# Kernel optimization log

Measured on AMD Instinct MI355X. Metric: run time of the kernel, lower is better.

Reference implementation:

```python
import jax, jax.numpy as jnp
import numpy as np
import math

N, NF, D, HEADS, LEVELS, POINTS = 1, 2, 256, 8, 4, 4
SPATIAL = np.array([[100, 100], [50, 50], [25, 25], [13, 13]], dtype=np.int32)
LEN_IN = int((SPATIAL[:, 0] * SPATIAL[:, 1]).sum())  # 13294
LEN_Q = LEN_IN


def _grid_init_bias():
    # faithful to MSDeformAttn._reset_parameters
    thetas = np.arange(HEADS, dtype=np.float32) * (2.0 * math.pi / HEADS)
    grid = np.stack([np.cos(thetas), np.sin(thetas)], -1)
    grid = grid / np.abs(grid).max(-1, keepdims=True)
    grid = np.tile(grid.reshape(HEADS, 1, 1, 2), (1, LEVELS, POINTS, 1))
    for i in range(POINTS):
        grid[:, :, i, :] *= i + 1
    return grid.reshape(-1).astype(np.float32)  # [HEADS*LEVELS*POINTS*2]


def setup_inputs() -> dict:
    key = jax.random.key(0)
    ks = jax.random.split(key, 8)
    lsi = np.concatenate([[0], np.cumsum(SPATIAL[:, 0] * SPATIAL[:, 1])[:-1]]).astype(np.int32)
    s = 1.0 / math.sqrt(D)
    return {
        "query": jax.random.normal(ks[0], (N, NF, LEN_Q, D), jnp.float32),
        "reference_points": jax.random.uniform(ks[1], (N, LEN_Q, LEVELS, 2), jnp.float32),
        "input_flatten": jax.random.normal(ks[2], (N, NF, LEN_IN, D), jnp.float32),
        "input_spatial_shapes": jnp.asarray(SPATIAL),
        "input_level_start_index": jnp.asarray(lsi),
        "Wv": jax.random.normal(ks[3], (D, D), jnp.float32) * s,
        "bv": jnp.zeros((D,), jnp.float32),
        "Woff": jax.random.normal(ks[4], (D, HEADS * LEVELS * POINTS * 2), jnp.float32) * 0.01,
        "boff": jnp.asarray(_grid_init_bias()),
        "Wattn": jax.random.normal(ks[5], (D, HEADS * LEVELS * POINTS), jnp.float32) * 0.02,
        "battn": jnp.zeros((HEADS * LEVELS * POINTS,), jnp.float32),
        "Wout": jax.random.normal(ks[6], (D, D), jnp.float32) * s,
        "bout": jnp.zeros((D,), jnp.float32),
    }


def ms_deform_attn_core(value, spatial_shapes, level_start_index, loc, attn):
    """value: [B, Lin, H, Dh]; loc: [B, Lq, H, L, P, 2] in [0,1]; attn: [B, Lq, H, L, P].
    Bilinear sampling matches F.grid_sample(align_corners=False, padding_mode='zeros')
    applied to grid = 2*loc - 1, i.e. pixel coord = loc*size - 0.5."""
    B, Lin, Hn, Dh = value.shape
    Lq, L, P = loc.shape[1], loc.shape[3], loc.shape[4]
    val_t = value.transpose(0, 2, 1, 3)  # [B, H, Lin, Dh]
    out = jnp.zeros((B, Lq, Hn, Dh), value.dtype)
    for l in range(L):
        Hl = spatial_shapes[l, 0]
        Wl = spatial_shapes[l, 1]
        start = level_start_index[l]
        x = loc[:, :, :, l, :, 0] * Wl - 0.5  # [B, Lq, H, P]
        y = loc[:, :, :, l, :, 1] * Hl - 0.5
        x0 = jnp.floor(x)
        y0 = jnp.floor(y)
        lx, ly = x - x0, y - y0
        x0i = x0.astype(jnp.int32)
        y0i = y0.astype(jnp.int32)
        sampled = jnp.zeros((B, Lq, Hn, P, Dh), value.dtype)
        corners = [(0, 0, (1 - lx) * (1 - ly)), (0, 1, lx * (1 - ly)),
                   (1, 0, (1 - lx) * ly), (1, 1, lx * ly)]
        for dy, dx, w in corners:
            xi = x0i + dx
            yi = y0i + dy
            valid = (xi >= 0) & (xi < Wl) & (yi >= 0) & (yi < Hl)
            idx = start + jnp.clip(yi, 0, Hl - 1) * Wl + jnp.clip(xi, 0, Wl - 1)
            idx_t = idx.transpose(0, 2, 1, 3).reshape(B, Hn, Lq * P)  # [B, H, Lq*P]
            v = jnp.take_along_axis(val_t, idx_t[:, :, :, None], axis=2)  # [B, H, Lq*P, Dh]
            v = v.reshape(B, Hn, Lq, P, Dh).transpose(0, 2, 1, 3, 4)  # [B, Lq, H, P, Dh]
            sampled = sampled + jnp.where(valid, w, 0.0)[..., None] * v
        out = out + jnp.einsum('blhp,blhpd->blhd', attn[:, :, :, l, :], sampled)
    return out.reshape(B, Lq, Hn * Dh)


def reference(query, reference_points, input_flatten, input_spatial_shapes,
              input_level_start_index, Wv, bv, Woff, boff, Wattn, battn, Wout, bout):
    n, nf, Lq, d = query.shape
    Lin = input_flatten.shape[2]
    Dh = d // HEADS
    value = (input_flatten @ Wv + bv).reshape(n * nf, Lin, HEADS, Dh)
    off = (query @ Woff + boff).reshape(n, nf, Lq, HEADS, LEVELS, POINTS, 2)
    aw = (query @ Wattn + battn).reshape(n, nf, Lq, HEADS, LEVELS * POINTS)
    aw = jax.nn.softmax(aw, axis=-1).reshape(n, nf, Lq, HEADS, LEVELS, POINTS)
    # offset normalizer: [W, H] per level
    norm = jnp.stack([input_spatial_shapes[:, 1], input_spatial_shapes[:, 0]], -1).astype(query.dtype)
    # reference_points: [n, Lq, L, 2] -> broadcast with offsets [n, nf, Lq, H, L, P, 2]
    loc = reference_points[:, None, :, None, :, None, :] + off / norm[None, None, None, None, :, None, :]
    loc = loc.reshape(n * nf, Lq, HEADS, LEVELS, POINTS, 2)
    aw = aw.reshape(n * nf, Lq, HEADS, LEVELS, POINTS)
    out = ms_deform_attn_core(value, input_spatial_shapes, input_level_start_index, loc, aw)
    out = out.reshape(n, nf, Lq, d)
    return out @ Wout + bout
```

## Files before the change

### kernel.cpp

```cpp
#include <hip/hip_runtime.h>
#include <math.h>

#define LEN_Q 13294
#define LEN_IN 13294
#define NFRAMES 2
#define MTOT (LEN_Q * NFRAMES)
#define HEADS 8
#define LEVELS 4
#define POINTS 4

typedef __attribute__((ext_vector_type(8))) short short8;
typedef __attribute__((ext_vector_type(4))) float f32x4;
typedef __attribute__((ext_vector_type(4))) int i32x4;
typedef __attribute__((ext_vector_type(2))) unsigned int uint2v;
typedef __attribute__((ext_vector_type(4))) unsigned int uint4v;
typedef __attribute__((ext_vector_type(4))) unsigned short ushort4v;

__device__ __forceinline__ unsigned short f2bf(float x) {
    unsigned u = __builtin_bit_cast(unsigned, x);
    unsigned r = (u + 0x7fffu + ((u >> 16) & 1u)) >> 16;
    return (unsigned short)r;
}
__device__ __forceinline__ float bf2f(unsigned short b) {
    return __builtin_bit_cast(float, (unsigned)b << 16);
}
__device__ __forceinline__ float bfl(unsigned u) {
    return __builtin_bit_cast(float, u << 16);
}
__device__ __forceinline__ float bfh(unsigned u) {
    return __builtin_bit_cast(float, u & 0xffff0000u);
}

#define LSTR 40

__global__ __launch_bounds__(256) void prep_weights(
    const float* __restrict__ Wv,  const float* __restrict__ Woff,
    const float* __restrict__ Wat, const float* __restrict__ Wout,
    unsigned short* __restrict__ wvT,
    unsigned short* __restrict__ woaT,
    unsigned short* __restrict__ woutT)
{
    const int b = blockIdx.x;
    const int k = threadIdx.x;
    const float* src; unsigned short* dst; int N; int n;
    if (b < 256)      { src = Wv;   dst = wvT;          N = 256; n = b; }
    else if (b < 512) { src = Woff; dst = woaT;         N = 256; n = b - 256; }
    else if (b < 640) { src = Wat;  dst = woaT + 65536; N = 128; n = b - 512; }
    else              { src = Wout; dst = woutT;        N = 256; n = b - 640; }
    dst[(size_t)n * 256 + k] = f2bf(src[(size_t)k * N + n]);
}

__global__ __launch_bounds__(256, 3) void gemm_fused(
    const float* __restrict__ Aval,
    const float* __restrict__ Aq,
    const unsigned short* __restrict__ BTv,
    const unsigned short* __restrict__ BToa,
    const float* __restrict__ bv,
    const float* __restrict__ boff,
    const float* __restrict__ battn,
    unsigned short* __restrict__ vdup,
    unsigned short* __restrict__ off16,
    unsigned short* __restrict__ at16,
    int M, int K)
{
    __shared__ unsigned short As[128 * LSTR];
    __shared__ unsigned short Bs[128 * LSTR];

    const int t = threadIdx.x;
    const int w = t >> 6;
    const int L = t & 63;
    const int m0 = blockIdx.y * 128;
    const bool isVal = (blockIdx.x < 2);
    const int nTile = isVal ? blockIdx.x : blockIdx.x - 2;
    const float* Af = isVal ? Aval : Aq;
    const unsigned short* BTb = (isVal ? BTv : BToa) + (size_t)nTile * 128 * K;

    const int sr = t >> 1;
    const int sc = (t & 1) * 16;
    int arow = m0 + sr; if (arow > M - 1) arow = M - 1;
    const float* Ag = Af + (size_t)arow * K + sc;
    const unsigned short* Bg = BTb + (size_t)sr * K + sc;
    unsigned short* AsW = &As[sr * LSTR + sc];
    unsigned short* BsW = &Bs[sr * LSTR + sc];

    const int mq = (w & 1) * 64;
    const int nq = (w >> 1) * 64;
    const int lr = L & 15;
    const int kq = (L >> 4) * 8;

    f32x4 acc[4][4];
    #pragma unroll
    for (int i = 0; i < 4; ++i)
        #pragma unroll
        for (int j = 0; j < 4; ++j) acc[i][j] = (f32x4){0.f, 0.f, 0.f, 0.f};

    f32x4 a0 = *(const f32x4*)(Ag);
    f32x4 a1 = *(const f32x4*)(Ag + 4);
    f32x4 a2 = *(const f32x4*)(Ag + 8);
    f32x4 a3 = *(const f32x4*)(Ag + 12);
    short8 b0 = *(const short8*)(Bg);
    short8 b1 = *(const short8*)(Bg + 8);

    for (int k0 = 0; k0 < K; k0 += 32) {
        short8 p0, p1;
        p0[0]=(short)f2bf(a0.x); p0[1]=(short)f2bf(a0.y); p0[2]=(short)f2bf(a0.z); p0[3]=(short)f2bf(a0.w);
        p0[4]=(short)f2bf(a1.x); p0[5]=(short)f2bf(a1.y); p0[6]=(short)f2bf(a1.z); p0[7]=(short)f2bf(a1.w);
        p1[0]=(short)f2bf(a2.x); p1[1]=(short)f2bf(a2.y); p1[2]=(short)f2bf(a2.z); p1[3]=(short)f2bf(a2.w);
        p1[4]=(short)f2bf(a3.x); p1[5]=(short)f2bf(a3.y); p1[6]=(short)f2bf(a3.z); p1[7]=(short)f2bf(a3.w);
        __syncthreads();
        *(short8*)(AsW) = p0;
        *(short8*)(AsW + 8) = p1;
        *(short8*)(BsW) = b0;
        *(short8*)(BsW + 8) = b1;
        __syncthreads();

        if (k0 + 32 < K) {
            a0 = *(const f32x4*)(Ag + k0 + 32);
            a1 = *(const f32x4*)(Ag + k0 + 36);
            a2 = *(const f32x4*)(Ag + k0 + 40);
            a3 = *(const f32x4*)(Ag + k0 + 44);
            b0 = *(const short8*)(Bg + k0 + 32);
            b1 = *(const short8*)(Bg + k0 + 40);
        }

        short8 af[4], bf[4];
        #pragma unroll
        for (int i = 0; i < 4; ++i)
            af[i] = *(const short8*)&As[(mq + i * 16 + lr) * LSTR + kq];
        #pragma unroll
        for (int j = 0; j < 4; ++j)
            bf[j] = *(const short8*)&Bs[(nq + j * 16 + lr) * LSTR + kq];
        #pragma unroll
        for (int i = 0; i < 4; ++i)
            #pragma unroll
            for (int j = 0; j < 4; ++j)
                acc[i][j] = __builtin_amdgcn_mfma_f32_16x16x32_bf16(af[i], bf[j], acc[i][j], 0, 0, 0);
    }

    const int rr = (L >> 4) * 4;
    #pragma unroll
    for (int i = 0; i < 4; ++i) {
        #pragma unroll
        for (int r = 0; r < 4; ++r) {
            int m = m0 + mq + i * 16 + rr + r;
            if (m < M) {
                #pragma unroll
                for (int j = 0; j < 4; ++j) {
                    int colg = nTile * 128 + nq + j * 16 + lr;
                    float v = acc[i][j][r];
                    if (isVal) {
                        int hh = colg >> 5, d = colg & 31;
                        int fr = (m >= LEN_Q) ? 1 : 0;
                        int e = m - fr * LEN_Q;
                        size_t ebase = ((size_t)(fr * 8 + hh) * (LEN_IN + 1) + e) * 64;
                        unsigned short bvv = f2bf(v + bv[colg]);
                        vdup[ebase + d] = bvv;
                        if (e > 0) vdup[ebase - 64 + 32 + d] = bvv;
                    } else if (colg < 256) {
                        off16[(size_t)m * 256 + colg] = f2bf(v + boff[colg]);
                    } else {
                        at16[(size_t)m * 128 + (colg - 256)] = f2bf(v + battn[colg - 256]);
                    }
                }
            }
        }
    }
}

__global__ __launch_bounds__(256, 3) void gemm_out(
    const unsigned short* __restrict__ A,
    const unsigned short* __restrict__ BT,
    const float* __restrict__ bias,
    float* __restrict__ C,
    int M, int K)
{
    __shared__ unsigned short As[128 * LSTR];
    __shared__ unsigned short Bs[128 * LSTR];

    const int t = threadIdx.x;
    const int w = t >> 6;
    const int L = t & 63;
    const int m0 = blockIdx.y * 128;
    const int n0 = blockIdx.x * 128;

    const int sr = t >> 1;
    const int sc = (t & 1) * 16;
    int arow = m0 + sr; if (arow > M - 1) arow = M - 1;
    const unsigned short* Ag = A + (size_t)arow * K + sc;
    const unsigned short* Bg = BT + (size_t)(n0 + sr) * K + sc;
    unsigned short* AsW = &As[sr * LSTR + sc];
    unsigned short* BsW = &Bs[sr * LSTR + sc];

    const int mq = (w & 1) * 64;
    const int nq = (w >> 1) * 64;
    const int lr = L & 15;
    const int kq = (L >> 4) * 8;

    f32x4 acc[4][4];
    #pragma unroll
    for (int i = 0; i < 4; ++i)
        #pragma unroll
        for (int j = 0; j < 4; ++j) acc[i][j] = (f32x4){0.f, 0.f, 0.f, 0.f};

    short8 a0 = *(const short8*)(Ag);
    short8 a1 = *(const short8*)(Ag + 8);
    short8 b0 = *(const short8*)(Bg);
    short8 b1 = *(const short8*)(Bg + 8);

    for (int k0 = 0; k0 < K; k0 += 32) {
        __syncthreads();
        *(short8*)(AsW) = a0;
        *(short8*)(AsW + 8) = a1;
        *(short8*)(BsW) = b0;
        *(short8*)(BsW + 8) = b1;
        __syncthreads();

        if (k0 + 32 < K) {
            a0 = *(const short8*)(Ag + k0 + 32);
            a1 = *(const short8*)(Ag + k0 + 40);
            b0 = *(const short8*)(Bg + k0 + 32);
            b1 = *(const short8*)(Bg + k0 + 40);
        }

        short8 af[4], bf[4];
        #pragma unroll
        for (int i = 0; i < 4; ++i)
            af[i] = *(const short8*)&As[(mq + i * 16 + lr) * LSTR + kq];
        #pragma unroll
        for (int j = 0; j < 4; ++j)
            bf[j] = *(const short8*)&Bs[(nq + j * 16 + lr) * LSTR + kq];
        #pragma unroll
        for (int i = 0; i < 4; ++i)
            #pragma unroll
            for (int j = 0; j < 4; ++j)
                acc[i][j] = __builtin_amdgcn_mfma_f32_16x16x32_bf16(af[i], bf[j], acc[i][j], 0, 0, 0);
    }

    const int rr = (L >> 4) * 4;
    #pragma unroll
    for (int i = 0; i < 4; ++i) {
        #pragma unroll
        for (int r = 0; r < 4; ++r) {
            int m = m0 + mq + i * 16 + rr + r;
            if (m < M) {
                #pragma unroll
                for (int j = 0; j < 4; ++j) {
                    int n = n0 + nq + j * 16 + lr;
                    C[(size_t)m * 256 + n] = acc[i][j][r] + bias[n];
                }
            }
        }
    }
}

__global__ __launch_bounds__(256) void sample10(
    const unsigned short* __restrict__ vdup,
    const unsigned short* __restrict__ off,
    const unsigned short* __restrict__ attn,
    const float* __restrict__ refpts,
    const int*   __restrict__ spatial,
    const int*   __restrict__ lsi,
    unsigned short* __restrict__ samp)
{
    const int b = blockIdx.x;
    const int h = b & 7;
    const int chunk = b >> 3;
    const int t = threadIdx.x;
    const int rl = t >> 3;
    const int j = t & 7;

    int row = chunk * 32 + rl;
    const bool valid = row < MTOT;
    if (row > MTOT - 1) row = MTOT - 1;
    const int frame = row >= LEN_Q ? 1 : 0;
    const int q = row - frame * LEN_Q;

    __shared__ float w_s[32][68];
    __shared__ int   b_s[32][20];

    uint2v ov = *(const uint2v*)(off + (size_t)row * 256 + h * 32 + j * 4);
    unsigned av = *(const unsigned*)(attn + (size_t)row * 128 + h * 16 + j * 2);
    float t0 = bf2f((unsigned short)(av & 0xffffu));
    float t1 = bf2f((unsigned short)(av >> 16));

    float m = fmaxf(t0, t1);
    #pragma unroll
    for (int d = 1; d < 8; d <<= 1) m = fmaxf(m, __shfl_xor(m, d));
    float e0 = __expf(t0 - m);
    float e1 = __expf(t1 - m);
    float s = e0 + e1;
    #pragma unroll
    for (int d = 1; d < 8; d <<= 1) s += __shfl_xor(s, d);
    float inv = 1.f / s;
    float wt01[2] = { e0 * inv, e1 * inv };

    {
        const int l = j >> 1;
        const int Hl = spatial[l * 2], Wl = spatial[l * 2 + 1];
        const int start = lsi[l];
        const int slab = (frame * 8 + h) * (LEN_IN + 1);
        const float rx = refpts[((size_t)q * LEVELS + l) * 2];
        const float ry = refpts[((size_t)q * LEVELS + l) * 2 + 1];
        #pragma unroll
        for (int i = 0; i < 2; ++i) {
            const int lp = 2 * j + i;
            unsigned sel = (i == 0) ? ov.x : ov.y;
            float ox = bf2f((unsigned short)(sel & 0xffffu));
            float oy = bf2f((unsigned short)(sel >> 16));
            float locx = rx + ox * __builtin_amdgcn_rcpf((float)Wl);
            float locy = ry + oy * __builtin_amdgcn_rcpf((float)Hl);
            float wt = wt01[i];
            float x = locx * (float)Wl - 0.5f;
            float y = locy * (float)Hl - 0.5f;
            float x0f = floorf(x), y0f = floorf(y);
            float lx = x - x0f, ly = y - y0f;
            int x0 = (int)x0f, y0 = (int)y0f;
            int xbase = min(max(x0, 0), Wl - 2);
            int ybase = min(max(y0, 0), Hl - 2);
            float wxe0 = (x0 == xbase) ? (1.f - lx) : ((x0 == -1) ? lx : 0.f);
            float wxe1 = (x0 == xbase) ? lx : ((x0 == Wl - 1) ? (1.f - lx) : 0.f);
            float wye0 = (y0 == ybase) ? (1.f - ly) : ((y0 == -1) ? ly : 0.f);
            float wye1 = (y0 == ybase) ? ly : ((y0 == Hl - 1) ? (1.f - ly) : 0.f);
            b_s[rl][lp] = (slab + start + ybase * Wl + xbase) * 128;
            f32x4 wv;
            wv.x = wt * wxe0 * wye0;
            wv.y = wt * wxe1 * wye0;
            wv.z = wt * wxe0 * wye1;
            wv.w = wt * wxe1 * wye1;
            *(f32x4*)&w_s[rl][lp * 4] = wv;
        }
    }
    __syncthreads();

    const char* vb = (const char*)vdup;
    const unsigned lane16 = (unsigned)(j * 16);
    const int hi = (j >> 2) & 1;
    int ystr[4];
    #pragma unroll
    for (int l2 = 0; l2 < 4; ++l2) ystr[l2] = spatial[l2 * 2 + 1] * 128;

    f32x4  wreg[2][2];
    uint4v vbuf[2][4];
    auto fetch = [&](int buf, int g) {
        wreg[buf][0] = *(const f32x4*)&w_s[rl][(2 * g) * 4];
        wreg[buf][1] = *(const f32x4*)&w_s[rl][(2 * g + 1) * 4];
        int b0 = b_s[rl][2 * g];
        int b1 = b_s[rl][2 * g + 1];
        int ys = ystr[g >> 1];
        vbuf[buf][0] = *(const uint4v*)(vb + (unsigned)b0 + lane16);
        vbuf[buf][1] = *(const uint4v*)(vb + (unsigned)(b0 + ys) + lane16);
        vbuf[buf][2] = *(const uint4v*)(vb + (unsigned)b1 + lane16);
        vbuf[buf][3] = *(const uint4v*)(vb + (unsigned)(b1 + ys) + lane16);
    };

    float a[8];
    #pragma unroll
    for (int k = 0; k < 8; ++k) a[k] = 0.f;

    fetch(0, 0);
    #pragma unroll
    for (int g = 0; g < 8; ++g) {
        const int cur = g & 1;
        if (g < 7) fetch(cur ^ 1, g + 1);
        #pragma unroll
        for (int p = 0; p < 2; ++p) {
            f32x4 w4 = wreg[cur][p];
            float wy0 = hi ? w4.y : w4.x;
            float wy1 = hi ? w4.w : w4.z;
            uint4v v0 = vbuf[cur][p * 2];
            uint4v v1 = vbuf[cur][p * 2 + 1];
            #pragma unroll
            for (int k = 0; k < 4; ++k) {
                unsigned u0 = v0[k], u1 = v1[k];
                a[2 * k]     = fmaf(wy0, bfl(u0), a[2 * k]);
                a[2 * k + 1] = fmaf(wy0, bfh(u0), a[2 * k + 1]);
                a[2 * k]     = fmaf(wy1, bfl(u1), a[2 * k]);
                a[2 * k + 1] = fmaf(wy1, bfh(u1), a[2 * k + 1]);
            }
        }
    }

    #pragma unroll
    for (int k = 0; k < 8; ++k) a[k] += __shfl_xor(a[k], 4);

    if (valid && hi == 0) {
        uint4v o;
        #pragma unroll
        for (int k = 0; k < 4; ++k)
            o[k] = (unsigned)f2bf(a[2 * k]) | ((unsigned)f2bf(a[2 * k + 1]) << 16);
        *(uint4v*)(samp + (size_t)row * 256 + h * 32 + (j & 3) * 8) = o;
    }
}

extern "C" void kernel_launch(void* const* d_in, const int* in_sizes, int n_in,
                              void* d_out, int out_size, void* d_ws, size_t ws_size,
                              hipStream_t stream)
{
    const float* query   = (const float*)d_in[0];
    const float* refpts  = (const float*)d_in[1];
    const float* inflat  = (const float*)d_in[2];
    const int*   spatial = (const int*)d_in[3];
    const int*   lsi     = (const int*)d_in[4];
    const float* Wv      = (const float*)d_in[5];
    const float* bv      = (const float*)d_in[6];
    const float* Woff    = (const float*)d_in[7];
    const float* boff    = (const float*)d_in[8];
    const float* Wattn   = (const float*)d_in[9];
    const float* battn   = (const float*)d_in[10];
    const float* Wout    = (const float*)d_in[11];
    const float* bout    = (const float*)d_in[12];

    unsigned short* ws = (unsigned short*)d_ws;
    const size_t MR = (size_t)MTOT * 256;
    const size_t VDUP = (size_t)16 * (LEN_IN + 1) * 64;
    unsigned short* vdup   = ws;
    unsigned short* off16  = vdup + VDUP;
    unsigned short* at16   = off16 + MR;
    unsigned short* samp16 = at16 + (size_t)MTOT * 128;
    unsigned short* wvT    = samp16 + MR;
    unsigned short* woaT   = wvT + 65536;
    unsigned short* woutT  = woaT + 98304;

    dim3 blk256(256);
    const int mBlocks = (MTOT + 127) / 128;

    hipLaunchKernelGGL(prep_weights, dim3(896), blk256, 0, stream,
                       Wv, Woff, Wattn, Wout, wvT, woaT, woutT);

    hipLaunchKernelGGL(gemm_fused, dim3(5, mBlocks), blk256, 0, stream,
                       inflat, query, wvT, woaT, bv, boff, battn,
                       vdup, off16, at16, MTOT, 256);

    hipLaunchKernelGGL(sample10, dim3(6648), blk256, 0, stream,
                       vdup, off16, at16, refpts, spatial, lsi, samp16);

    hipLaunchKernelGGL(gemm_out, dim3(2, mBlocks), blk256, 0, stream,
                       samp16, woutT, bout, (float*)d_out, MTOT, 256);
}
```

Before: 207.2 us.

## Stage full-K A row panel in LDS and stream B from global in GEMMs

```diff
diff --git a/kernel.cpp b/kernel.cpp
--- a/kernel.cpp
+++ b/kernel.cpp
@@ -11,10 +11,8 @@
 
 typedef __attribute__((ext_vector_type(8))) short short8;
 typedef __attribute__((ext_vector_type(4))) float f32x4;
-typedef __attribute__((ext_vector_type(4))) int i32x4;
 typedef __attribute__((ext_vector_type(2))) unsigned int uint2v;
 typedef __attribute__((ext_vector_type(4))) unsigned int uint4v;
-typedef __attribute__((ext_vector_type(4))) unsigned short ushort4v;
 
 __device__ __forceinline__ unsigned short f2bf(float x) {
     unsigned u = __builtin_bit_cast(unsigned, x);
@@ -30,8 +28,14 @@
 __device__ __forceinline__ float bfh(unsigned u) {
     return __builtin_bit_cast(float, u & 0xffff0000u);
 }
-
-#define LSTR 40
+__device__ __forceinline__ short8 pack8(f32x4 x0, f32x4 x1) {
+    short8 p;
+    p[0]=(short)f2bf(x0.x); p[1]=(short)f2bf(x0.y); p[2]=(short)f2bf(x0.z); p[3]=(short)f2bf(x0.w);
+    p[4]=(short)f2bf(x1.x); p[5]=(short)f2bf(x1.y); p[6]=(short)f2bf(x1.z); p[7]=(short)f2bf(x1.w);
+    return p;
+}
+
+#define ASTR 264
 
 __global__ __launch_bounds__(256) void prep_weights(
     const float* __restrict__ Wv,  const float* __restrict__ Woff,
@@ -50,7 +54,7 @@
     dst[(size_t)n * 256 + k] = f2bf(src[(size_t)k * N + n]);
 }
 
-__global__ __launch_bounds__(256, 3) void gemm_fused(
+__global__ __launch_bounds__(256, 2) void gemm_fused2(
     const float* __restrict__ Aval,
     const float* __restrict__ Aq,
     const unsigned short* __restrict__ BTv,
@@ -61,105 +65,97 @@
     unsigned short* __restrict__ vdup,
     unsigned short* __restrict__ off16,
     unsigned short* __restrict__ at16,
-    int M, int K)
+    int M)
 {
-    __shared__ unsigned short As[128 * LSTR];
-    __shared__ unsigned short Bs[128 * LSTR];
+    __shared__ unsigned short Asv[64 * ASTR];
+    __shared__ unsigned short Asq[64 * ASTR];
 
     const int t = threadIdx.x;
     const int w = t >> 6;
     const int L = t & 63;
-    const int m0 = blockIdx.y * 128;
-    const bool isVal = (blockIdx.x < 2);
-    const int nTile = isVal ? blockIdx.x : blockIdx.x - 2;
-    const float* Af = isVal ? Aval : Aq;
-    const unsigned short* BTb = (isVal ? BTv : BToa) + (size_t)nTile * 128 * K;
-
-    const int sr = t >> 1;
-    const int sc = (t & 1) * 16;
-    int arow = m0 + sr; if (arow > M - 1) arow = M - 1;
-    const float* Ag = Af + (size_t)arow * K + sc;
-    const unsigned short* Bg = BTb + (size_t)sr * K + sc;
-    unsigned short* AsW = &As[sr * LSTR + sc];
-    unsigned short* BsW = &Bs[sr * LSTR + sc];
-
-    const int mq = (w & 1) * 64;
+    const int m0 = blockIdx.x * 64;
+
+    {
+        const int r = t >> 2;
+        const int c0 = (t & 3) * 64;
+        int arow = m0 + r; if (arow > M - 1) arow = M - 1;
+        const float* pv = Aval + (size_t)arow * 256 + c0;
+        const float* pq = Aq   + (size_t)arow * 256 + c0;
+        unsigned short* dv = &Asv[r * ASTR + c0];
+        unsigned short* dq = &Asq[r * ASTR + c0];
+        #pragma unroll
+        for (int cc = 0; cc < 64; cc += 16) {
+            f32x4 v0 = *(const f32x4*)(pv + cc);
+            f32x4 v1 = *(const f32x4*)(pv + cc + 4);
+            f32x4 v2 = *(const f32x4*)(pv + cc + 8);
+            f32x4 v3 = *(const f32x4*)(pv + cc + 12);
+            f32x4 q0 = *(const f32x4*)(pq + cc);
+            f32x4 q1 = *(const f32x4*)(pq + cc + 4);
+            f32x4 q2 = *(const f32x4*)(pq + cc + 8);
+            f32x4 q3 = *(const f32x4*)(pq + cc + 12);
+            *(short8*)(dv + cc)     = pack8(v0, v1);
+            *(short8*)(dv + cc + 8) = pack8(v2, v3);
+            *(short8*)(dq + cc)     = pack8(q0, q1);
+            *(short8*)(dq + cc + 8) = pack8(q2, q3);
+        }
+    }
+    __syncthreads();
+
+    const int mq = (w & 1) * 32;
     const int nq = (w >> 1) * 64;
     const int lr = L & 15;
     const int kq = (L >> 4) * 8;
-
-    f32x4 acc[4][4];
-    #pragma unroll
-    for (int i = 0; i < 4; ++i)
-        #pragma unroll
-        for (int j = 0; j < 4; ++j) acc[i][j] = (f32x4){0.f, 0.f, 0.f, 0.f};
-
-    f32x4 a0 = *(const f32x4*)(Ag);
-    f32x4 a1 = *(const f32x4*)(Ag + 4);
-    f32x4 a2 = *(const f32x4*)(Ag + 8);
-    f32x4 a3 = *(const f32x4*)(Ag + 12);
-    short8 b0 = *(const short8*)(Bg);
-    short8 b1 = *(const short8*)(Bg + 8);
-
-    for (int k0 = 0; k0 < K; k0 += 32) {
-        short8 p0, p1;
-        p0[0]=(short)f2bf(a0.x); p0[1]=(short)f2bf(a0.y); p0[2]=(short)f2bf(a0.z); p0[3]=(short)f2bf(a0.w);
-        p0[4]=(short)f2bf(a1.x); p0[5]=(short)f2bf(a1.y); p0[6]=(short)f2bf(a1.z); p0[7]=(short)f2bf(a1.w);
-        p1[0]=(short)f2bf(a2.x); p1[1]=(short)f2bf(a2.y); p1[2]=(short)f2bf(a2.z); p1[3]=(short)f2bf(a2.w);
-        p1[4]=(short)f2bf(a3.x); p1[5]=(short)f2bf(a3.y); p1[6]=(short)f2bf(a3.z); p1[7]=(short)f2bf(a3.w);
-        __syncthreads();
-        *(short8*)(AsW) = p0;
-        *(short8*)(AsW + 8) = p1;
-        *(short8*)(BsW) = b0;
-        *(short8*)(BsW + 8) = b1;
-        __syncthreads();
-
-        if (k0 + 32 < K) {
-            a0 = *(const f32x4*)(Ag + k0 + 32);
-            a1 = *(const f32x4*)(Ag + k0 + 36);
-            a2 = *(const f32x4*)(Ag + k0 + 40);
-            a3 = *(const f32x4*)(Ag + k0 + 44);
-            b0 = *(const short8*)(Bg + k0 + 32);
-            b1 = *(const short8*)(Bg + k0 + 40);
-        }
-
-        short8 af[4], bf[4];
-        #pragma unroll
-        for (int i = 0; i < 4; ++i)
-            af[i] = *(const short8*)&As[(mq + i * 16 + lr) * LSTR + kq];
-        #pragma unroll
-        for (int j = 0; j < 4; ++j)
-            bf[j] = *(const short8*)&Bs[(nq + j * 16 + lr) * LSTR + kq];
-        #pragma unroll
-        for (int i = 0; i < 4; ++i)
+    const int rr = (L >> 4) * 4;
+
+    for (int nt = 0; nt < 5; ++nt) {
+        const unsigned short* As = (nt < 2) ? Asv : Asq;
+        const unsigned short* BTb = (nt < 2) ? (BTv + (size_t)nt * 128 * 256)
+                                             : (BToa + (size_t)(nt - 2) * 128 * 256);
+        f32x4 acc[2][4];
+        #pragma unroll
+        for (int i = 0; i < 2; ++i)
+            #pragma unroll
+            for (int j = 0; j < 4; ++j) acc[i][j] = (f32x4){0.f, 0.f, 0.f, 0.f};
+
+        #pragma unroll
+        for (int k0 = 0; k0 < 256; k0 += 32) {
+            short8 af[2], bf[4];
+            #pragma unroll
+            for (int i = 0; i < 2; ++i)
+                af[i] = *(const short8*)&As[(mq + i * 16 + lr) * ASTR + k0 + kq];
             #pragma unroll
             for (int j = 0; j < 4; ++j)
-                acc[i][j] = __builtin_amdgcn_mfma_f32_16x16x32_bf16(af[i], bf[j], acc[i][j], 0, 0, 0);
-    }
-
-    const int rr = (L >> 4) * 4;
-    #pragma unroll
-    for (int i = 0; i < 4; ++i) {
-        #pragma unroll
-        for (int r = 0; r < 4; ++r) {
-            int m = m0 + mq + i * 16 + rr + r;
-            if (m < M) {
+                bf[j] = *(const short8*)&BTb[(size_t)(nq + j * 16 + lr) * 256 + k0 + kq];
+            #pragma unroll
+            for (int i = 0; i < 2; ++i)
                 #pragma unroll
-                for (int j = 0; j < 4; ++j) {
-                    int colg = nTile * 128 + nq + j * 16 + lr;
-                    float v = acc[i][j][r];
-                    if (isVal) {
-                        int hh = colg >> 5, d = colg & 31;
-                        int fr = (m >= LEN_Q) ? 1 : 0;
-                        int e = m - fr * LEN_Q;
-                        size_t ebase = ((size_t)(fr * 8 + hh) * (LEN_IN + 1) + e) * 64;
-                        unsigned short bvv = f2bf(v + bv[colg]);
-                        vdup[ebase + d] = bvv;
-                        if (e > 0) vdup[ebase - 64 + 32 + d] = bvv;
-                    } else if (colg < 256) {
-                        off16[(size_t)m * 256 + colg] = f2bf(v + boff[colg]);
-                    } else {
-                        at16[(size_t)m * 128 + (colg - 256)] = f2bf(v + battn[colg - 256]);
+                for (int j = 0; j < 4; ++j)
+                    acc[i][j] = __builtin_amdgcn_mfma_f32_16x16x32_bf16(af[i], bf[j], acc[i][j], 0, 0, 0);
+        }
+
+        #pragma unroll
+        for (int i = 0; i < 2; ++i) {
+            #pragma unroll
+            for (int r = 0; r < 4; ++r) {
+                int m = m0 + mq + i * 16 + rr + r;
+                if (m < M) {
+                    #pragma unroll
+                    for (int j = 0; j < 4; ++j) {
+                        int colg = nt * 128 + nq + j * 16 + lr;
+                        float vacc = acc[i][j][r];
+                        if (colg < 256) {
+                            int hh = colg >> 5, d = colg & 31;
+                            int fr = (m >= LEN_Q) ? 1 : 0;
+                            int e = m - fr * LEN_Q;
+                            size_t ebase = ((size_t)(fr * 8 + hh) * (LEN_IN + 1) + e) * 64;
+                            unsigned short bvv = f2bf(vacc + bv[colg]);
+                            vdup[ebase + d] = bvv;
+                            if (e > 0) vdup[ebase - 64 + 32 + d] = bvv;
+                        } else {
+                            int oa = colg - 256;
+                            if (oa < 256) off16[(size_t)m * 256 + oa] = f2bf(vacc + boff[oa]);
+                            else          at16[(size_t)m * 128 + (oa - 256)] = f2bf(vacc + battn[oa - 256]);
+                        }
                     }
                 }
             }
@@ -167,86 +163,73 @@
     }
 }
 
-__global__ __launch_bounds__(256, 3) void gemm_out(
+__global__ __launch_bounds__(256, 4) void gemm_out2(
     const unsigned short* __restrict__ A,
     const unsigned short* __restrict__ BT,
     const float* __restrict__ bias,
     float* __restrict__ C,
-    int M, int K)
+    int M)
 {
-    __shared__ unsigned short As[128 * LSTR];
-    __shared__ unsigned short Bs[128 * LSTR];
+    __shared__ unsigned short As[64 * ASTR];
 
     const int t = threadIdx.x;
     const int w = t >> 6;
     const int L = t & 63;
-    const int m0 = blockIdx.y * 128;
-    const int n0 = blockIdx.x * 128;
-
-    const int sr = t >> 1;
-    const int sc = (t & 1) * 16;
-    int arow = m0 + sr; if (arow > M - 1) arow = M - 1;
-    const unsigned short* Ag = A + (size_t)arow * K + sc;
-    const unsigned short* Bg = BT + (size_t)(n0 + sr) * K + sc;
-    unsigned short* AsW = &As[sr * LSTR + sc];
-    unsigned short* BsW = &Bs[sr * LSTR + sc];
-
-    const int mq = (w & 1) * 64;
+    const int m0 = blockIdx.x * 64;
+
+    {
+        const int r = t >> 2;
+        const int c0 = (t & 3) * 64;
+        int arow = m0 + r; if (arow > M - 1) arow = M - 1;
+        const unsigned short* pa = A + (size_t)arow * 256 + c0;
+        unsigned short* da = &As[r * ASTR + c0];
+        #pragma unroll
+        for (int cc = 0; cc < 64; cc += 8)
+            *(short8*)(da + cc) = *(const short8*)(pa + cc);
+    }
+    __syncthreads();
+
+    const int mq = (w & 1) * 32;
     const int nq = (w >> 1) * 64;
     const int lr = L & 15;
     const int kq = (L >> 4) * 8;
-
-    f32x4 acc[4][4];
-    #pragma unroll
-    for (int i = 0; i < 4; ++i)
-        #pragma unroll
-        for (int j = 0; j < 4; ++j) acc[i][j] = (f32x4){0.f, 0.f, 0.f, 0.f};
-
-    short8 a0 = *(const short8*)(Ag);
-    short8 a1 = *(const short8*)(Ag + 8);
-    short8 b0 = *(const short8*)(Bg);
-    short8 b1 = *(const short8*)(Bg + 8);
-
-    for (int k0 = 0; k0 < K; k0 += 32) {
-        __syncthreads();
-        *(short8*)(AsW) = a0;
-        *(short8*)(AsW + 8) = a1;
-        *(short8*)(BsW) = b0;
-        *(short8*)(BsW + 8) = b1;
-        __syncthreads();
-
-        if (k0 + 32 < K) {
-            a0 = *(const short8*)(Ag + k0 + 32);
-            a1 = *(const short8*)(Ag + k0 + 40);
-            b0 = *(const short8*)(Bg + k0 + 32);
-            b1 = *(const short8*)(Bg + k0 + 40);
-        }
-
-        short8 af[4], bf[4];
-        #pragma unroll
-        for (int i = 0; i < 4; ++i)
-            af[i] = *(const short8*)&As[(mq + i * 16 + lr) * LSTR + kq];
-        #pragma unroll
-        for (int j = 0; j < 4; ++j)
-            bf[j] = *(const short8*)&Bs[(nq + j * 16 + lr) * LSTR + kq];
-        #pragma unroll
-        for (int i = 0; i < 4; ++i)
+    const int rr = (L >> 4) * 4;
+
+    for (int nt = 0; nt < 2; ++nt) {
+        const unsigned short* BTb = BT + (size_t)nt * 128 * 256;
+        f32x4 acc[2][4];
+        #pragma unroll
+        for (int i = 0; i < 2; ++i)
+            #pragma unroll
+            for (int j = 0; j < 4; ++j) acc[i][j] = (f32x4){0.f, 0.f, 0.f, 0.f};
+
+        #pragma unroll
+        for (int k0 = 0; k0 < 256; k0 += 32) {
+            short8 af[2], bf[4];
+            #pragma unroll
+            for (int i = 0; i < 2; ++i)
+                af[i] = *(const short8*)&As[(mq + i * 16 + lr) * ASTR + k0 + kq];
             #pragma unroll
             for (int j = 0; j < 4; ++j)
-                acc[i][j] = __builtin_amdgcn_mfma_f32_16x16x32_bf16(af[i], bf[j], acc[i][j], 0, 0, 0);
-    }
-
-    const int rr = (L >> 4) * 4;
-    #pragma unroll
-    for (int i = 0; i < 4; ++i) {
-        #pragma unroll
-        for (int r = 0; r < 4; ++r) {
-            int m = m0 + mq + i * 16 + rr + r;
-            if (m < M) {
+                bf[j] = *(const short8*)&BTb[(size_t)(nq + j * 16 + lr) * 256 + k0 + kq];
+            #pragma unroll
+            for (int i = 0; i < 2; ++i)
                 #pragma unroll
-                for (int j = 0; j < 4; ++j) {
-                    int n = n0 + nq + j * 16 + lr;
-                    C[(size_t)m * 256 + n] = acc[i][j][r] + bias[n];
+                for (int j = 0; j < 4; ++j)
+                    acc[i][j] = __builtin_amdgcn_mfma_f32_16x16x32_bf16(af[i], bf[j], acc[i][j], 0, 0, 0);
+        }
+
+        #pragma unroll
+        for (int i = 0; i < 2; ++i) {
+            #pragma unroll
+            for (int r = 0; r < 4; ++r) {
+                int m = m0 + mq + i * 16 + rr + r;
+                if (m < M) {
+                    #pragma unroll
+                    for (int j = 0; j < 4; ++j) {
+                        int n = nt * 128 + nq + j * 16 + lr;
+                        C[(size_t)m * 256 + n] = acc[i][j][r] + bias[n];
+                    }
                 }
             }
         }
@@ -422,18 +405,18 @@
     unsigned short* woutT  = woaT + 98304;
 
     dim3 blk256(256);
-    const int mBlocks = (MTOT + 127) / 128;
+    const int mBlocks64 = (MTOT + 63) / 64;
 
     hipLaunchKernelGGL(prep_weights, dim3(896), blk256, 0, stream,
                        Wv, Woff, Wattn, Wout, wvT, woaT, woutT);
 
-    hipLaunchKernelGGL(gemm_fused, dim3(5, mBlocks), blk256, 0, stream,
+    hipLaunchKernelGGL(gemm_fused2, dim3(mBlocks64), blk256, 0, stream,
                        inflat, query, wvT, woaT, bv, boff, battn,
-                       vdup, off16, at16, MTOT, 256);
+                       vdup, off16, at16, MTOT);
 
     hipLaunchKernelGGL(sample10, dim3(6648), blk256, 0, stream,
                        vdup, off16, at16, refpts, spatial, lsi, samp16);
 
-    hipLaunchKernelGGL(gemm_out, dim3(2, mBlocks), blk256, 0, stream,
-                       samp16, woutT, bout, (float*)d_out, MTOT, 256);
-}
+    hipLaunchKernelGGL(gemm_out2, dim3(mBlocks64), blk256, 0, stream,
+                       samp16, woutT, bout, (float*)d_out, MTOT);
+}
```

New measurement: 258.4 us. 24.7% more time.
